# Kernel tuning notes

Hardware: AMD Instinct MI355X
Metric: run time of the kernel (lower is better)

## Reference

```python
import math
import jax, jax.numpy as jnp
import numpy as np

IN_CH = 512
KEY = 512
VAL = 512
B, T = 8, 2048
SQRT_KEY = math.sqrt(float(KEY))


def setup_inputs() -> dict:
    key = jax.random.key(0)
    ks = jax.random.split(key, 7)
    s_in = 1.0 / math.sqrt(IN_CH)
    return {
        "x": jax.random.normal(ks[0], (B, T, IN_CH), dtype=jnp.float32),
        "Wq": jax.random.uniform(ks[1], (IN_CH, KEY), jnp.float32, -s_in, s_in),
        "bq": jax.random.uniform(ks[2], (KEY,), jnp.float32, -s_in, s_in),
        "Wk": jax.random.uniform(ks[3], (IN_CH, KEY), jnp.float32, -s_in, s_in),
        "bk": jax.random.uniform(ks[4], (KEY,), jnp.float32, -s_in, s_in),
        "Wv": jax.random.uniform(ks[5], (IN_CH, VAL), jnp.float32, -s_in, s_in),
        "bv": jax.random.uniform(ks[6], (VAL,), jnp.float32, -s_in, s_in),
    }


def reference(x, Wq, bq, Wk, bk, Wv, bv):
    # x: [B, T, C]
    q = x @ Wq + bq          # [B, T, K]
    k = x @ Wk + bk          # [B, T, K]
    v = x @ Wv + bv          # [B, T, V]
    logits = jnp.einsum("btk,bsk->bts", q, k)  # [B, T(q), T(kv)]
    mask = jnp.tril(jnp.ones((T, T), dtype=bool))  # causal: key s <= query t
    logits = jnp.where(mask[None, :, :], logits, -jnp.inf)
    # NOTE: original torch code softmaxes over dim=1 (the QUERY axis) — kept faithful.
    probs = jax.nn.softmax(logits / SQRT_KEY, axis=1)
    read = jnp.einsum("bts,bsv->btv", probs, v)  # [B, T, V]
    return jnp.concatenate((x, read), axis=2)    # [B, T, C+V]
```

## Files before the change

kernel.cpp:

```cpp
#include <hip/hip_runtime.h>
#include <hip/hip_bf16.h>
#include <math.h>

#define BATCH 8
#define SEQ   2048
#define CH    512
#define ROWS  (BATCH * SEQ)
#define INVSQ 0.044194173824159216f

#define TP 68

typedef __attribute__((ext_vector_type(8))) __bf16 bf16x8;
typedef __attribute__((ext_vector_type(4))) float f32x4;

__device__ inline unsigned short f2bf(float f) {
    unsigned u = __builtin_bit_cast(unsigned, f);
    u += 0x7fffu + ((u >> 16) & 1u);
    return (unsigned short)(u >> 16);
}
__device__ inline float bf2f(unsigned short s) {
    unsigned u = ((unsigned)s) << 16;
    return __builtin_bit_cast(float, u);
}

__global__ __launch_bounds__(256) void fuse_x_kernel(
    const float* __restrict__ x, unsigned short* __restrict__ xb,
    float* __restrict__ out, float* __restrict__ Z)
{
    if (blockIdx.x < 64) Z[blockIdx.x * 256 + threadIdx.x] = 0.f;
    size_t base = ((size_t)blockIdx.x * 256 + threadIdx.x) * 8;
    size_t row = base >> 9, c = base & 511;
    float4 v0 = *(const float4*)(x + base);
    float4 v1 = *(const float4*)(x + base + 4);
    float* o = out + row * 1024 + c;
    *(float4*)o = v0;
    *(float4*)(o + 4) = v1;
    alignas(16) unsigned short t[8];
    t[0] = f2bf(v0.x); t[1] = f2bf(v0.y); t[2] = f2bf(v0.z); t[3] = f2bf(v0.w);
    t[4] = f2bf(v1.x); t[5] = f2bf(v1.y); t[6] = f2bf(v1.z); t[7] = f2bf(v1.w);
    *(uint4*)(xb + base) = *(const uint4*)t;
}

__global__ __launch_bounds__(256) void transpose_w_kernel(
    const float* __restrict__ Wq, const float* __restrict__ Wk,
    const float* __restrict__ Wv, unsigned short* __restrict__ Wt)
{
    __shared__ unsigned short T[64 * TP];
    const int k0 = blockIdx.x * 64, n0 = blockIdx.y * 64, w = blockIdx.z;
    const float* W = (w == 0) ? Wq : (w == 1) ? Wk : Wv;
    const int tid = threadIdx.x;
#pragma unroll
    for (int i = 0; i < 2; ++i) {
        int slot = tid + i * 256;
        int kr = slot >> 3, c8 = (slot & 7) << 3;
        float4 a = *(const float4*)(W + (size_t)(k0 + kr) * CH + n0 + c8);
        float4 b = *(const float4*)(W + (size_t)(k0 + kr) * CH + n0 + c8 + 4);
        T[(c8 + 0) * TP + kr] = f2bf(a.x); T[(c8 + 1) * TP + kr] = f2bf(a.y);
        T[(c8 + 2) * TP + kr] = f2bf(a.z); T[(c8 + 3) * TP + kr] = f2bf(a.w);
        T[(c8 + 4) * TP + kr] = f2bf(b.x); T[(c8 + 5) * TP + kr] = f2bf(b.y);
        T[(c8 + 6) * TP + kr] = f2bf(b.z); T[(c8 + 7) * TP + kr] = f2bf(b.w);
    }
    __syncthreads();
#pragma unroll
    for (int i = 0; i < 2; ++i) {
        int slot = tid + i * 256;
        int nr = slot >> 3, k8 = (slot & 7) << 3;
        uint2 lo = *(const uint2*)(T + nr * TP + k8);
        uint2 hi = *(const uint2*)(T + nr * TP + k8 + 4);
        uint4 u; u.x = lo.x; u.y = lo.y; u.z = hi.x; u.w = hi.y;
        *(uint4*)(Wt + ((size_t)w * CH + n0 + nr) * CH + k0 + k8) = u;
    }
}

__global__ __launch_bounds__(256) void transpose_v_kernel(
    const unsigned short* __restrict__ vb, const float* __restrict__ Z,
    unsigned short* __restrict__ Vt)
{
    __shared__ unsigned short T[64 * TP];
    const int s0 = blockIdx.x * 64, v0 = blockIdx.y * 64, b = blockIdx.z;
    const int tid = threadIdx.x;
#pragma unroll
    for (int i = 0; i < 2; ++i) {
        int slot = tid + i * 256;
        int sr = slot >> 3, c8 = (slot & 7) << 3;
        float inv = 1.0f / Z[b * SEQ + s0 + sr];
        uint4 raw = *(const uint4*)(vb + ((size_t)b * SEQ + s0 + sr) * CH + v0 + c8);
        const unsigned short* p = (const unsigned short*)&raw;
#pragma unroll
        for (int j = 0; j < 8; ++j)
            T[(c8 + j) * TP + sr] = f2bf(bf2f(p[j]) * inv);
    }
    __syncthreads();
#pragma unroll
    for (int i = 0; i < 2; ++i) {
        int slot = tid + i * 256;
        int vr = slot >> 3, s8 = (slot & 7) << 3;
        uint2 lo = *(const uint2*)(T + vr * TP + s8);
        uint2 hi = *(const uint2*)(T + vr * TP + s8 + 4);
        uint4 u; u.x = lo.x; u.y = lo.y; u.z = hi.x; u.w = hi.y;
        *(uint4*)(Vt + ((size_t)b * CH + v0 + vr) * SEQ + s0 + s8) = u;
    }
}

#define FRAG_READS                                                            \
    bf16x8 a0[4], a1[4], c0[4], c1[4];                                        \
    _Pragma("unroll")                                                         \
    for (int rr = 0; rr < 4; ++rr) {                                          \
        const unsigned short* ap = Ab + (arow + rr * 16) * 64;                \
        const unsigned short* bp = Bb + (brow + rr * 16) * 64;                \
        a0[rr] = *(const bf16x8*)(ap + s80);                                  \
        a1[rr] = *(const bf16x8*)(ap + s81);                                  \
        c0[rr] = *(const bf16x8*)(bp + s80);                                  \
        c1[rr] = *(const bf16x8*)(bp + s81);                                  \
    }

#define MFMA_TILE                                                             \
    _Pragma("unroll")                                                         \
    for (int rr = 0; rr < 4; ++rr)                                            \
        _Pragma("unroll")                                                     \
        for (int cc = 0; cc < 4; ++cc)                                        \
            acc[rr][cc] = __builtin_amdgcn_mfma_f32_16x16x32_bf16(            \
                a0[rr], c0[cc], acc[rr][cc], 0, 0, 0);                        \
    _Pragma("unroll")                                                         \
    for (int rr = 0; rr < 4; ++rr)                                            \
        _Pragma("unroll")                                                     \
        for (int cc = 0; cc < 4; ++cc)                                        \
            acc[rr][cc] = __builtin_amdgcn_mfma_f32_16x16x32_bf16(            \
                a1[rr], c1[cc], acc[rr][cc], 0, 0, 0);

#define STAGE4(gsrc, dslab)                                                   \
    _Pragma("unroll")                                                         \
    for (int p = 0; p < 4; ++p)                                               \
        __builtin_amdgcn_global_load_lds(                                     \
            (const __attribute__((address_space(1))) unsigned int*)((gsrc) + (size_t)p * 32 * gstride), \
            (__attribute__((address_space(3))) unsigned int*)((dslab) + p * 2048 + (tid << 3)), \
            16, 0, 0);

#define PIPE_PROLOGUE                                                         \
    stageA(0); stageB(0); stageB(1);                                          \
    asm volatile("s_waitcnt vmcnt(4)" ::: "memory");                          \
    __builtin_amdgcn_s_barrier();                                             \
    __builtin_amdgcn_sched_barrier(0);

#define PIPE_BODY(NTv)                                                        \
    {                                                                         \
        const unsigned short* Ab = lds + (U & 1) * 8192;                      \
        const unsigned short* Bb = lds + 16384 + (U & 1) * 8192;              \
        stageA(U + 1);                                                        \
        FRAG_READS                                                            \
        asm volatile("s_waitcnt lgkmcnt(0)" ::: "memory");                    \
        __builtin_amdgcn_s_barrier();                                         \
        __builtin_amdgcn_sched_barrier(0);                                    \
        stageB(U + 2);                                                        \
        __builtin_amdgcn_s_setprio(1);                                        \
        MFMA_TILE                                                             \
        __builtin_amdgcn_s_setprio(0);                                        \
        if (U <= (NTv) - 3)      asm volatile("s_waitcnt vmcnt(4)" ::: "memory"); \
        else if (U == (NTv) - 2) asm volatile("s_waitcnt vmcnt(0)" ::: "memory"); \
        __builtin_amdgcn_s_barrier();                                         \
        __builtin_amdgcn_sched_barrier(0);                                    \
    }

__global__ __launch_bounds__(256, 2) void qkv8_kernel(
    const unsigned short* __restrict__ xb, const unsigned short* __restrict__ Wt,
    const float* __restrict__ bq, const float* __restrict__ bk,
    const float* __restrict__ bv, unsigned short* __restrict__ qkv)
{
    __shared__ unsigned short lds[32768];
    const int tid = threadIdx.x;
    const int lane = tid & 63, wave = tid >> 6;
    const int waveA = wave >> 1;
    const int waveB = wave & 1;
    const int quad = lane >> 4, l16 = lane & 15;

    int id = (int)blockIdx.x;
    id = (id & 7) * 192 + (id >> 3);
    const int xt = id / 12, wt = id - xt * 12;
    const int xrow0 = xt << 7, wrow0 = wt << 7;

    const size_t gstride = CH;
    const unsigned short* __restrict__ Wg = Wt + (size_t)wrow0 * CH;
    const unsigned short* __restrict__ Xg = xb + (size_t)xrow0 * CH;

    const int scol = (((tid & 7) ^ ((tid >> 3) & 7)) << 3);
    const size_t ga = (size_t)(tid >> 3) * gstride + scol;
    const int s80 = ((quad ^ (l16 & 7)) << 3);
    const int s81 = s80 ^ 32;
    const int arow = waveA * 64 + l16;
    const int brow = waveB * 64 + l16;

    f32x4 acc[4][4] = {};

    auto stageA = [&](int V) {
        if (V >= 8) return;
        const unsigned short* g = Wg + ga + V * 64;
        unsigned short* d = lds + (V & 1) * 8192;
        STAGE4(g, d)
    };
    auto stageB = [&](int V) {
        if (V >= 8) return;
        const unsigned short* g = Xg + ga + V * 64;
        unsigned short* d = lds + 16384 + (V & 1) * 8192;
        STAGE4(g, d)
    };

    PIPE_PROLOGUE
#pragma unroll
    for (int U = 0; U < 8; ++U) PIPE_BODY(8)

    const int which = wrow0 >> 9;
    const float* bias = (which == 0) ? bq : (which == 1) ? bk : bv;
    const float scale = (which == 0) ? INVSQ : 1.0f;
    unsigned short* outw = qkv + (size_t)which * ROWS * CH;
    const int colblk = wrow0 & 511;
#pragma unroll
    for (int r = 0; r < 4; ++r) {
        int colb = colblk + waveA * 64 + r * 16 + quad * 4;
        float4 b4 = *(const float4*)(bias + colb);
#pragma unroll
        for (int c = 0; c < 4; ++c) {
            int m = xrow0 + waveB * 64 + c * 16 + l16;
            alignas(8) unsigned short pk[4];
            pk[0] = f2bf((acc[r][c][0] + b4.x) * scale);
            pk[1] = f2bf((acc[r][c][1] + b4.y) * scale);
            pk[2] = f2bf((acc[r][c][2] + b4.z) * scale);
            pk[3] = f2bf((acc[r][c][3] + b4.w) * scale);
            *(uint2*)(outw + (size_t)m * CH + colb) = *(const uint2*)pk;
        }
    }
}

__global__ __launch_bounds__(256, 2) void logits8_kernel(
    const unsigned short* __restrict__ qb, const unsigned short* __restrict__ kb,
    unsigned short* __restrict__ E, float* __restrict__ Z)
{
    __shared__ unsigned short lds[32768];
    const int tid = threadIdx.x;
    const int lane = tid & 63, wave = tid >> 6;
    const int waveA = wave >> 1;
    const int waveB = wave & 1;
    const int quad = lane >> 4, l16 = lane & 15;

    const int b = (int)blockIdx.x & 7;
    const int i = (int)blockIdx.x >> 3;
    int tt = (int)((sqrtf(8.f * (float)i + 1.f) - 1.f) * 0.5f);
    int st = i - ((tt * (tt + 1)) >> 1);
    while (st < 0)  { --tt; st = i - ((tt * (tt + 1)) >> 1); }
    while (st > tt) { ++tt; st = i - ((tt * (tt + 1)) >> 1); }
    const int m0s = st << 7;
    const int n0t = tt << 7;

    const size_t gstride = CH;
    const unsigned short* __restrict__ Ag = kb + ((size_t)b * SEQ + m0s) * CH;
    const unsigned short* __restrict__ Bg = qb + ((size_t)b * SEQ + n0t) * CH;

    const int scol = (((tid & 7) ^ ((tid >> 3) & 7)) << 3);
    const size_t ga = (size_t)(tid >> 3) * gstride + scol;
    const int s80 = ((quad ^ (l16 & 7)) << 3);
    const int s81 = s80 ^ 32;
    const int arow = waveA * 64 + l16;
    const int brow = waveB * 64 + l16;

    f32x4 acc[4][4] = {};

    auto stageA = [&](int V) {
        if (V >= 8) return;
        const unsigned short* g = Ag + ga + V * 64;
        unsigned short* d = lds + (V & 1) * 8192;
        STAGE4(g, d)
    };
    auto stageB = [&](int V) {
        if (V >= 8) return;
        const unsigned short* g = Bg + ga + V * 64;
        unsigned short* d = lds + 16384 + (V & 1) * 8192;
        STAGE4(g, d)
    };

    PIPE_PROLOGUE
#pragma unroll
    for (int U = 0; U < 8; ++U) PIPE_BODY(8)

#pragma unroll
    for (int r = 0; r < 4; ++r) {
        int sb = m0s + waveA * 64 + r * 16 + quad * 4;
        float ev[4][4];
#pragma unroll
        for (int c = 0; c < 4; ++c) {
            int t = n0t + waveB * 64 + c * 16 + l16;
#pragma unroll
            for (int reg = 0; reg < 4; ++reg)
                ev[c][reg] = (sb + reg <= t) ? __expf(acc[r][c][reg]) : 0.f;
        }
#pragma unroll
        for (int reg = 0; reg < 4; ++reg) {
            float z = ev[0][reg] + ev[1][reg] + ev[2][reg] + ev[3][reg];
            z += __shfl_xor(z, 1);
            z += __shfl_xor(z, 2);
            z += __shfl_xor(z, 4);
            z += __shfl_xor(z, 8);
            if (l16 == 0) atomicAdd(&Z[b * SEQ + sb + reg], z);
        }
#pragma unroll
        for (int c = 0; c < 4; ++c) {
            int t = n0t + waveB * 64 + c * 16 + l16;
            alignas(8) unsigned short pk[4];
            pk[0] = f2bf(ev[c][0]); pk[1] = f2bf(ev[c][1]);
            pk[2] = f2bf(ev[c][2]); pk[3] = f2bf(ev[c][3]);
            *(uint2*)(E + ((size_t)b * SEQ + t) * SEQ + sb) = *(const uint2*)pk;
        }
    }
}

__global__ __launch_bounds__(256, 2) void read8_kernel(
    const unsigned short* __restrict__ E, const unsigned short* __restrict__ Vt,
    float* __restrict__ out)
{
    __shared__ unsigned short lds[32768];
    const int tid = threadIdx.x;
    const int lane = tid & 63, wave = tid >> 6;
    const int waveA = wave >> 1;
    const int waveB = wave & 1;
    const int quad = lane >> 4, l16 = lane & 15;

    const int id = blockIdx.x;
    const int b = id & 7;
    const int rem = id >> 3;
    const int mv = rem & 3;
    const int r0 = rem >> 2;
    const int tt = (r0 < 8) ? r0 : 23 - r0;
    const int m0v = mv << 7;
    const int n0t = tt << 7;
    const int NT = (tt + 1) * 2;

    const size_t gstride = SEQ;
    const unsigned short* __restrict__ Ag = Vt + ((size_t)b * CH + m0v) * SEQ;
    const unsigned short* __restrict__ Bg = E + ((size_t)b * SEQ + n0t) * SEQ;

    const int scol = (((tid & 7) ^ ((tid >> 3) & 7)) << 3);
    const size_t ga = (size_t)(tid >> 3) * gstride + scol;
    const int s80 = ((quad ^ (l16 & 7)) << 3);
    const int s81 = s80 ^ 32;
    const int arow = waveA * 64 + l16;
    const int brow = waveB * 64 + l16;

    f32x4 acc[4][4] = {};

    auto stageA = [&](int V) {
        if (V >= NT) return;
        const unsigned short* g = Ag + ga + V * 64;
        unsigned short* d = lds + (V & 1) * 8192;
        STAGE4(g, d)
    };
    auto stageB = [&](int V) {
        if (V >= NT) return;
        const unsigned short* g = Bg + ga + V * 64;
        unsigned short* d = lds + 16384 + (V & 1) * 8192;
        STAGE4(g, d)
    };

    PIPE_PROLOGUE
#pragma unroll 2
    for (int U = 0; U < NT; ++U) PIPE_BODY(NT)

#pragma unroll
    for (int r = 0; r < 4; ++r) {
        int v = 512 + m0v + waveA * 64 + r * 16 + quad * 4;
#pragma unroll
        for (int c = 0; c < 4; ++c) {
            int t = n0t + waveB * 64 + c * 16 + l16;
            float4 f;
            f.x = acc[r][c][0]; f.y = acc[r][c][1];
            f.z = acc[r][c][2]; f.w = acc[r][c][3];
            *(float4*)(out + ((size_t)b * SEQ + t) * 1024 + v) = f;
        }
    }
}

extern "C" void kernel_launch(void* const* d_in, const int* in_sizes, int n_in,
                              void* d_out, int out_size, void* d_ws, size_t ws_size,
                              hipStream_t stream) {
    const float* x  = (const float*)d_in[0];
    const float* Wq = (const float*)d_in[1];
    const float* bq = (const float*)d_in[2];
    const float* Wk = (const float*)d_in[3];
    const float* bk = (const float*)d_in[4];
    const float* Wv = (const float*)d_in[5];
    const float* bv = (const float*)d_in[6];
    float* out = (float*)d_out;

    char* ws = (char*)d_ws;
    const size_t QKV_BYTES = (size_t)ROWS * CH * 2;
    const size_t E_BYTES   = (size_t)BATCH * SEQ * SEQ * 2;
    unsigned short* qkv = (unsigned short*)ws;
    unsigned short* qb = qkv;
    unsigned short* kb = (unsigned short*)(ws + QKV_BYTES);
    unsigned short* vb = (unsigned short*)(ws + 2 * QKV_BYTES);
    unsigned short* E  = (unsigned short*)(ws + 3 * QKV_BYTES);
    float* Z = (float*)(ws + 3 * QKV_BYTES + E_BYTES);
    unsigned short* xb = E;
    unsigned short* Wt = (unsigned short*)((char*)E + QKV_BYTES);
    unsigned short* Vt = qb;

    dim3 blk(256);
    fuse_x_kernel<<<dim3(4096), blk, 0, stream>>>(x, xb, out, Z);
    transpose_w_kernel<<<dim3(8, 8, 3), blk, 0, stream>>>(Wq, Wk, Wv, Wt);
    qkv8_kernel<<<dim3(1536), blk, 0, stream>>>(xb, Wt, bq, bk, bv, qkv);
    logits8_kernel<<<dim3(1088), blk, 0, stream>>>(qb, kb, E, Z);
    transpose_v_kernel<<<dim3(32, 8, 8), blk, 0, stream>>>(vb, Z, Vt);
    read8_kernel<<<dim3(512), blk, 0, stream>>>(E, Vt, out);
}
```

Before: 213.9 us.

## Triple-buffer B operand in LDS and drop mid-iteration barrier in GEMM pipeline

The B operand staging buffer goes from two LDS slots to three (indexed by U % 3) in all three GEMM kernels. This lets stageB(U+2) be issued at the top of each iteration without overwriting data still being read, so the mid-iteration s_barrier can be removed. Fragment reads are split into two halves with a partial lgkmcnt wait, so the first half of the MFMAs can start while the second-half LDS reads are still in flight. The cost is more LDS per block (64KB to 80KB), which could limit occupancy, and modulo-3 indexing.

```diff
diff --git a/kernel.cpp b/kernel.cpp
--- a/kernel.cpp
+++ b/kernel.cpp
@@ -102,32 +102,6 @@
     }
 }
 
-#define FRAG_READS                                                            \
-    bf16x8 a0[4], a1[4], c0[4], c1[4];                                        \
-    _Pragma("unroll")                                                         \
-    for (int rr = 0; rr < 4; ++rr) {                                          \
-        const unsigned short* ap = Ab + (arow + rr * 16) * 64;                \
-        const unsigned short* bp = Bb + (brow + rr * 16) * 64;                \
-        a0[rr] = *(const bf16x8*)(ap + s80);                                  \
-        a1[rr] = *(const bf16x8*)(ap + s81);                                  \
-        c0[rr] = *(const bf16x8*)(bp + s80);                                  \
-        c1[rr] = *(const bf16x8*)(bp + s81);                                  \
-    }
-
-#define MFMA_TILE                                                             \
-    _Pragma("unroll")                                                         \
-    for (int rr = 0; rr < 4; ++rr)                                            \
-        _Pragma("unroll")                                                     \
-        for (int cc = 0; cc < 4; ++cc)                                        \
-            acc[rr][cc] = __builtin_amdgcn_mfma_f32_16x16x32_bf16(            \
-                a0[rr], c0[cc], acc[rr][cc], 0, 0, 0);                        \
-    _Pragma("unroll")                                                         \
-    for (int rr = 0; rr < 4; ++rr)                                            \
-        _Pragma("unroll")                                                     \
-        for (int cc = 0; cc < 4; ++cc)                                        \
-            acc[rr][cc] = __builtin_amdgcn_mfma_f32_16x16x32_bf16(            \
-                a1[rr], c1[cc], acc[rr][cc], 0, 0, 0);
-
 #define STAGE4(gsrc, dslab)                                                   \
     _Pragma("unroll")                                                         \
     for (int p = 0; p < 4; ++p)                                               \
@@ -145,15 +119,40 @@
 #define PIPE_BODY(NTv)                                                        \
     {                                                                         \
         const unsigned short* Ab = lds + (U & 1) * 8192;                      \
-        const unsigned short* Bb = lds + 16384 + (U & 1) * 8192;              \
+        const unsigned short* Bb = lds + 16384 + (U % 3) * 8192;              \
         stageA(U + 1);                                                        \
-        FRAG_READS                                                            \
+        stageB(U + 2);                                                        \
+        bf16x8 a0[4], a1[4], c0[4], c1[4];                                    \
+        _Pragma("unroll")                                                     \
+        for (int rr = 0; rr < 4; ++rr) {                                      \
+            a0[rr] = *(const bf16x8*)(Ab + (arow + rr * 16) * 64 + s80);      \
+            c0[rr] = *(const bf16x8*)(Bb + (brow + rr * 16) * 64 + s80);      \
+        }                                                                     \
+        __builtin_amdgcn_sched_barrier(0);                                    \
+        _Pragma("unroll")                                                     \
+        for (int rr = 0; rr < 4; ++rr) {                                      \
+            a1[rr] = *(const bf16x8*)(Ab + (arow + rr * 16) * 64 + s81);      \
+            c1[rr] = *(const bf16x8*)(Bb + (brow + rr * 16) * 64 + s81);      \
+        }                                                                     \
+        asm volatile("s_waitcnt lgkmcnt(8)" ::: "memory");                    \
+        __builtin_amdgcn_sched_barrier(0);                                    \
+        __builtin_amdgcn_s_setprio(1);                                        \
+        _Pragma("unroll")                                                     \
+        for (int rr = 0; rr < 4; ++rr)                                        \
+            _Pragma("unroll")                                                 \
+            for (int cc = 0; cc < 4; ++cc)                                    \
+                acc[rr][cc] = __builtin_amdgcn_mfma_f32_16x16x32_bf16(        \
+                    a0[rr], c0[cc], acc[rr][cc], 0, 0, 0);                    \
+        __builtin_amdgcn_s_setprio(0);                                        \
         asm volatile("s_waitcnt lgkmcnt(0)" ::: "memory");                    \
-        __builtin_amdgcn_s_barrier();                                         \
         __builtin_amdgcn_sched_barrier(0);                                    \
-        stageB(U + 2);                                                        \
         __builtin_amdgcn_s_setprio(1);                                        \
-        MFMA_TILE                                                             \
+        _Pragma("unroll")                                                     \
+        for (int rr = 0; rr < 4; ++rr)                                        \
+            _Pragma("unroll")                                                 \
+            for (int cc = 0; cc < 4; ++cc)                                    \
+                acc[rr][cc] = __builtin_amdgcn_mfma_f32_16x16x32_bf16(        \
+                    a1[rr], c1[cc], acc[rr][cc], 0, 0, 0);                    \
         __builtin_amdgcn_s_setprio(0);                                        \
         if (U <= (NTv) - 3)      asm volatile("s_waitcnt vmcnt(4)" ::: "memory"); \
         else if (U == (NTv) - 2) asm volatile("s_waitcnt vmcnt(0)" ::: "memory"); \
@@ -166,7 +165,7 @@
     const float* __restrict__ bq, const float* __restrict__ bk,
     const float* __restrict__ bv, unsigned short* __restrict__ qkv)
 {
-    __shared__ unsigned short lds[32768];
+    __shared__ unsigned short lds[40960];
     const int tid = threadIdx.x;
     const int lane = tid & 63, wave = tid >> 6;
     const int waveA = wave >> 1;
@@ -200,7 +199,7 @@
     auto stageB = [&](int V) {
         if (V >= 8) return;
         const unsigned short* g = Xg + ga + V * 64;
-        unsigned short* d = lds + 16384 + (V & 1) * 8192;
+        unsigned short* d = lds + 16384 + (V % 3) * 8192;
         STAGE4(g, d)
     };
 
@@ -234,7 +233,7 @@
     const unsigned short* __restrict__ qb, const unsigned short* __restrict__ kb,
     unsigned short* __restrict__ E, float* __restrict__ Z)
 {
-    __shared__ unsigned short lds[32768];
+    __shared__ unsigned short lds[40960];
     const int tid = threadIdx.x;
     const int lane = tid & 63, wave = tid >> 6;
     const int waveA = wave >> 1;
@@ -272,7 +271,7 @@
     auto stageB = [&](int V) {
         if (V >= 8) return;
         const unsigned short* g = Bg + ga + V * 64;
-        unsigned short* d = lds + 16384 + (V & 1) * 8192;
+        unsigned short* d = lds + 16384 + (V % 3) * 8192;
         STAGE4(g, d)
     };
 
@@ -315,7 +314,7 @@
     const unsigned short* __restrict__ E, const unsigned short* __restrict__ Vt,
     float* __restrict__ out)
 {
-    __shared__ unsigned short lds[32768];
+    __shared__ unsigned short lds[40960];
     const int tid = threadIdx.x;
     const int lane = tid & 63, wave = tid >> 6;
     const int waveA = wave >> 1;
@@ -354,7 +353,7 @@
     auto stageB = [&](int V) {
         if (V >= NT) return;
         const unsigned short* g = Bg + ga + V * 64;
-        unsigned short* d = lds + 16384 + (V & 1) * 8192;
+        unsigned short* d = lds + 16384 + (V % 3) * 8192;
         STAGE4(g, d)
     };
 
```

Measured after the change: 214.3 us. Within noise of the previous version (+0.2%).

## Enlarge QKV and logits GEMM tiles to 256x256 with 8 waves

Applied to the files above, without the earlier changes.

The qkv and logits GEMM kernels move from 128x128 tiles with 4 waves to 256x256 tiles with 512 threads and 8 waves. Each wave now owns a 128x64 output, and the inner loop is split into four MFMA sub-steps with barriers between them. This raises arithmetic intensity and cuts block count, at the cost of 128KB of LDS, more accumulator registers and more barriers per K step. The read kernel gets a triple-buffered B stage and split fragment reads with partial lgkmcnt waits, so MFMAs can start before all LDS reads finish.

```diff
diff --git a/kernel.cpp b/kernel.cpp
--- a/kernel.cpp
+++ b/kernel.cpp
@@ -102,111 +102,126 @@
     }
 }
 
-#define FRAG_READS                                                            \
-    bf16x8 a0[4], a1[4], c0[4], c1[4];                                        \
-    _Pragma("unroll")                                                         \
-    for (int rr = 0; rr < 4; ++rr) {                                          \
-        const unsigned short* ap = Ab + (arow + rr * 16) * 64;                \
-        const unsigned short* bp = Bb + (brow + rr * 16) * 64;                \
-        a0[rr] = *(const bf16x8*)(ap + s80);                                  \
-        a1[rr] = *(const bf16x8*)(ap + s81);                                  \
-        c0[rr] = *(const bf16x8*)(bp + s80);                                  \
-        c1[rr] = *(const bf16x8*)(bp + s81);                                  \
-    }
-
-#define MFMA_TILE                                                             \
-    _Pragma("unroll")                                                         \
-    for (int rr = 0; rr < 4; ++rr)                                            \
-        _Pragma("unroll")                                                     \
-        for (int cc = 0; cc < 4; ++cc)                                        \
-            acc[rr][cc] = __builtin_amdgcn_mfma_f32_16x16x32_bf16(            \
-                a0[rr], c0[cc], acc[rr][cc], 0, 0, 0);                        \
-    _Pragma("unroll")                                                         \
-    for (int rr = 0; rr < 4; ++rr)                                            \
-        _Pragma("unroll")                                                     \
-        for (int cc = 0; cc < 4; ++cc)                                        \
-            acc[rr][cc] = __builtin_amdgcn_mfma_f32_16x16x32_bf16(            \
-                a1[rr], c1[cc], acc[rr][cc], 0, 0, 0);
-
 #define STAGE4(gsrc, dslab)                                                   \
     _Pragma("unroll")                                                         \
     for (int p = 0; p < 4; ++p)                                               \
         __builtin_amdgcn_global_load_lds(                                     \
-            (const __attribute__((address_space(1))) unsigned int*)((gsrc) + (size_t)p * 32 * gstride), \
-            (__attribute__((address_space(3))) unsigned int*)((dslab) + p * 2048 + (tid << 3)), \
+            (const __attribute__((address_space(1))) unsigned int*)((gsrc) + (size_t)p * 64 * gstride), \
+            (__attribute__((address_space(3))) unsigned int*)((dslab) + p * 4096 + (tid << 3)), \
             16, 0, 0);
 
-#define PIPE_PROLOGUE                                                         \
-    stageA(0); stageB(0); stageB(1);                                          \
-    asm volatile("s_waitcnt vmcnt(4)" ::: "memory");                          \
+#define RD_A(rb)                                                              \
+    a00 = *(const bf16x8*)(Ab + (arow + (rb)     * 16) * 64 + s80);           \
+    a01 = *(const bf16x8*)(Ab + (arow + (rb)     * 16) * 64 + s81);           \
+    a10 = *(const bf16x8*)(Ab + (arow + (rb + 1) * 16) * 64 + s80);           \
+    a11 = *(const bf16x8*)(Ab + (arow + (rb + 1) * 16) * 64 + s81);
+
+#define MFMA_PAIR(rb)                                                         \
+    __builtin_amdgcn_s_setprio(1);                                            \
+    _Pragma("unroll")                                                         \
+    for (int cc = 0; cc < 4; ++cc)                                            \
+        acc[rb][cc] = __builtin_amdgcn_mfma_f32_16x16x32_bf16(a00, b0[cc], acc[rb][cc], 0, 0, 0); \
+    _Pragma("unroll")                                                         \
+    for (int cc = 0; cc < 4; ++cc)                                            \
+        acc[(rb) + 1][cc] = __builtin_amdgcn_mfma_f32_16x16x32_bf16(a10, b0[cc], acc[(rb) + 1][cc], 0, 0, 0); \
+    _Pragma("unroll")                                                         \
+    for (int cc = 0; cc < 4; ++cc)                                            \
+        acc[rb][cc] = __builtin_amdgcn_mfma_f32_16x16x32_bf16(a01, b1[cc], acc[rb][cc], 0, 0, 0); \
+    _Pragma("unroll")                                                         \
+    for (int cc = 0; cc < 4; ++cc)                                            \
+        acc[(rb) + 1][cc] = __builtin_amdgcn_mfma_f32_16x16x32_bf16(a11, b1[cc], acc[(rb) + 1][cc], 0, 0, 0); \
+    __builtin_amdgcn_s_setprio(0);
+
+#define BAR_LGKM                                                              \
     __builtin_amdgcn_s_barrier();                                             \
+    asm volatile("s_waitcnt lgkmcnt(0)" ::: "memory");                        \
     __builtin_amdgcn_sched_barrier(0);
 
-#define PIPE_BODY(NTv)                                                        \
-    {                                                                         \
-        const unsigned short* Ab = lds + (U & 1) * 8192;                      \
-        const unsigned short* Bb = lds + 16384 + (U & 1) * 8192;              \
+#define PIPE256(NT)                                                           \
+    stageA(0); stageB(0);                                                     \
+    asm volatile("s_waitcnt vmcnt(0)" ::: "memory");                          \
+    __builtin_amdgcn_s_barrier();                                             \
+    __builtin_amdgcn_sched_barrier(0);                                        \
+    _Pragma("unroll")                                                         \
+    for (int U = 0; U < (NT); ++U) {                                          \
+        const unsigned short* Ab = lds + (U & 1) * 16384;                     \
+        const unsigned short* Bb = lds + 32768 + (U & 1) * 16384;             \
+        bf16x8 b0[4], b1[4], a00, a01, a10, a11;                              \
+                                                            \
         stageA(U + 1);                                                        \
-        FRAG_READS                                                            \
-        asm volatile("s_waitcnt lgkmcnt(0)" ::: "memory");                    \
+        _Pragma("unroll")                                                     \
+        for (int n = 0; n < 4; ++n) {                                         \
+            b0[n] = *(const bf16x8*)(Bb + (brow + n * 16) * 64 + s80);        \
+            b1[n] = *(const bf16x8*)(Bb + (brow + n * 16) * 64 + s81);        \
+        }                                                                     \
+        RD_A(0)                                                               \
+        BAR_LGKM                                                              \
+        MFMA_PAIR(0)                                                          \
+        __builtin_amdgcn_s_barrier();                                         \
+                                                            \
+        stageB(U + 1);                                                        \
+        RD_A(2)                                                               \
+        BAR_LGKM                                                              \
+        MFMA_PAIR(2)                                                          \
+        __builtin_amdgcn_s_barrier();                                         \
+                                                            \
+        RD_A(4)                                                               \
+        BAR_LGKM                                                              \
+        MFMA_PAIR(4)                                                          \
+        __builtin_amdgcn_s_barrier();                                         \
+                                                            \
+        RD_A(6)                                                               \
+        BAR_LGKM                                                              \
+        MFMA_PAIR(6)                                                          \
+        if (U <= (NT) - 2) asm volatile("s_waitcnt vmcnt(0)" ::: "memory");   \
         __builtin_amdgcn_s_barrier();                                         \
         __builtin_amdgcn_sched_barrier(0);                                    \
-        stageB(U + 2);                                                        \
-        __builtin_amdgcn_s_setprio(1);                                        \
-        MFMA_TILE                                                             \
-        __builtin_amdgcn_s_setprio(0);                                        \
-        if (U <= (NTv) - 3)      asm volatile("s_waitcnt vmcnt(4)" ::: "memory"); \
-        else if (U == (NTv) - 2) asm volatile("s_waitcnt vmcnt(0)" ::: "memory"); \
-        __builtin_amdgcn_s_barrier();                                         \
-        __builtin_amdgcn_sched_barrier(0);                                    \
-    }
-
-__global__ __launch_bounds__(256, 2) void qkv8_kernel(
+    }
+
+__global__ __launch_bounds__(512) void qkv8_kernel(
     const unsigned short* __restrict__ xb, const unsigned short* __restrict__ Wt,
     const float* __restrict__ bq, const float* __restrict__ bk,
     const float* __restrict__ bv, unsigned short* __restrict__ qkv)
 {
-    __shared__ unsigned short lds[32768];
+    __shared__ unsigned short lds[65536];
     const int tid = threadIdx.x;
     const int lane = tid & 63, wave = tid >> 6;
-    const int waveA = wave >> 1;
-    const int waveB = wave & 1;
+    const int waveA = wave >> 2;
+    const int waveB = wave & 3;
     const int quad = lane >> 4, l16 = lane & 15;
 
     int id = (int)blockIdx.x;
-    id = (id & 7) * 192 + (id >> 3);
-    const int xt = id / 12, wt = id - xt * 12;
-    const int xrow0 = xt << 7, wrow0 = wt << 7;
+    id = (id & 7) * 48 + (id >> 3);
+    const int xt = id / 6, wt = id - xt * 6;
+    const int xrow0 = xt << 8, wrow0 = wt << 8;
 
     const size_t gstride = CH;
-    const unsigned short* __restrict__ Wg = Wt + (size_t)wrow0 * CH;
-    const unsigned short* __restrict__ Xg = xb + (size_t)xrow0 * CH;
+    const unsigned short* __restrict__ Ag = Wt + (size_t)wrow0 * CH;
+    const unsigned short* __restrict__ Bg = xb + (size_t)xrow0 * CH;
 
     const int scol = (((tid & 7) ^ ((tid >> 3) & 7)) << 3);
     const size_t ga = (size_t)(tid >> 3) * gstride + scol;
     const int s80 = ((quad ^ (l16 & 7)) << 3);
     const int s81 = s80 ^ 32;
-    const int arow = waveA * 64 + l16;
+    const int arow = waveA * 128 + l16;
     const int brow = waveB * 64 + l16;
 
-    f32x4 acc[4][4] = {};
+    f32x4 acc[8][4] = {};
 
     auto stageA = [&](int V) {
         if (V >= 8) return;
-        const unsigned short* g = Wg + ga + V * 64;
-        unsigned short* d = lds + (V & 1) * 8192;
+        const unsigned short* g = Ag + ga + V * 64;
+        unsigned short* d = lds + (V & 1) * 16384;
         STAGE4(g, d)
     };
     auto stageB = [&](int V) {
         if (V >= 8) return;
-        const unsigned short* g = Xg + ga + V * 64;
-        unsigned short* d = lds + 16384 + (V & 1) * 8192;
+        const unsigned short* g = Bg + ga + V * 64;
+        unsigned short* d = lds + 32768 + (V & 1) * 16384;
         STAGE4(g, d)
     };
 
-    PIPE_PROLOGUE
-#pragma unroll
-    for (int U = 0; U < 8; ++U) PIPE_BODY(8)
+    PIPE256(8)
 
     const int which = wrow0 >> 9;
     const float* bias = (which == 0) ? bq : (which == 1) ? bk : bv;
@@ -214,8 +229,8 @@
     unsigned short* outw = qkv + (size_t)which * ROWS * CH;
     const int colblk = wrow0 & 511;
 #pragma unroll
-    for (int r = 0; r < 4; ++r) {
-        int colb = colblk + waveA * 64 + r * 16 + quad * 4;
+    for (int r = 0; r < 8; ++r) {
+        int colb = colblk + waveA * 128 + r * 16 + quad * 4;
         float4 b4 = *(const float4*)(bias + colb);
 #pragma unroll
         for (int c = 0; c < 4; ++c) {
@@ -230,15 +245,15 @@
     }
 }
 
-__global__ __launch_bounds__(256, 2) void logits8_kernel(
+__global__ __launch_bounds__(512) void logits8_kernel(
     const unsigned short* __restrict__ qb, const unsigned short* __restrict__ kb,
     unsigned short* __restrict__ E, float* __restrict__ Z)
 {
-    __shared__ unsigned short lds[32768];
+    __shared__ unsigned short lds[65536];
     const int tid = threadIdx.x;
     const int lane = tid & 63, wave = tid >> 6;
-    const int waveA = wave >> 1;
-    const int waveB = wave & 1;
+    const int waveA = wave >> 2;
+    const int waveB = wave & 3;
     const int quad = lane >> 4, l16 = lane & 15;
 
     const int b = (int)blockIdx.x & 7;
@@ -247,8 +262,8 @@
     int st = i - ((tt * (tt + 1)) >> 1);
     while (st < 0)  { --tt; st = i - ((tt * (tt + 1)) >> 1); }
     while (st > tt) { ++tt; st = i - ((tt * (tt + 1)) >> 1); }
-    const int m0s = st << 7;
-    const int n0t = tt << 7;
+    const int m0s = st << 8;
+    const int n0t = tt << 8;
 
     const size_t gstride = CH;
     const unsigned short* __restrict__ Ag = kb + ((size_t)b * SEQ + m0s) * CH;
@@ -258,31 +273,29 @@
     const size_t ga = (size_t)(tid >> 3) * gstride + scol;
     const int s80 = ((quad ^ (l16 & 7)) << 3);
     const int s81 = s80 ^ 32;
-    const int arow = waveA * 64 + l16;
+    const int arow = waveA * 128 + l16;
     const int brow = waveB * 64 + l16;
 
-    f32x4 acc[4][4] = {};
+    f32x4 acc[8][4] = {};
 
     auto stageA = [&](int V) {
         if (V >= 8) return;
         const unsigned short* g = Ag + ga + V * 64;
-        unsigned short* d = lds + (V & 1) * 8192;
+        unsigned short* d = lds + (V & 1) * 16384;
         STAGE4(g, d)
     };
     auto stageB = [&](int V) {
         if (V >= 8) return;
         const unsigned short* g = Bg + ga + V * 64;
-        unsigned short* d = lds + 16384 + (V & 1) * 8192;
+        unsigned short* d = lds + 32768 + (V & 1) * 16384;
         STAGE4(g, d)
     };
 
-    PIPE_PROLOGUE
-#pragma unroll
-    for (int U = 0; U < 8; ++U) PIPE_BODY(8)
-
-#pragma unroll
-    for (int r = 0; r < 4; ++r) {
-        int sb = m0s + waveA * 64 + r * 16 + quad * 4;
+    PIPE256(8)
+
+#pragma unroll
+    for (int r = 0; r < 8; ++r) {
+        int sb = m0s + waveA * 128 + r * 16 + quad * 4;
         float ev[4][4];
 #pragma unroll
         for (int c = 0; c < 4; ++c) {
@@ -311,11 +324,19 @@
     }
 }
 
+#define R_STAGE4(gsrc, dslab)                                                 \
+    _Pragma("unroll")                                                         \
+    for (int p = 0; p < 4; ++p)                                               \
+        __builtin_amdgcn_global_load_lds(                                     \
+            (const __attribute__((address_space(1))) unsigned int*)((gsrc) + (size_t)p * 32 * gstride), \
+            (__attribute__((address_space(3))) unsigned int*)((dslab) + p * 2048 + (tid << 3)), \
+            16, 0, 0);
+
 __global__ __launch_bounds__(256, 2) void read8_kernel(
     const unsigned short* __restrict__ E, const unsigned short* __restrict__ Vt,
     float* __restrict__ out)
 {
-    __shared__ unsigned short lds[32768];
+    __shared__ unsigned short lds[40960];
     const int tid = threadIdx.x;
     const int lane = tid & 63, wave = tid >> 6;
     const int waveA = wave >> 1;
@@ -349,18 +370,63 @@
         if (V >= NT) return;
         const unsigned short* g = Ag + ga + V * 64;
         unsigned short* d = lds + (V & 1) * 8192;
-        STAGE4(g, d)
+        R_STAGE4(g, d)
     };
     auto stageB = [&](int V) {
         if (V >= NT) return;
         const unsigned short* g = Bg + ga + V * 64;
-        unsigned short* d = lds + 16384 + (V & 1) * 8192;
-        STAGE4(g, d)
-    };
-
-    PIPE_PROLOGUE
+        unsigned short* d = lds + 16384 + (V % 3) * 8192;
+        R_STAGE4(g, d)
+    };
+
+    stageA(0); stageB(0); stageB(1);
+    asm volatile("s_waitcnt vmcnt(4)" ::: "memory");
+    __builtin_amdgcn_s_barrier();
+    __builtin_amdgcn_sched_barrier(0);
+
 #pragma unroll 2
-    for (int U = 0; U < NT; ++U) PIPE_BODY(NT)
+    for (int U = 0; U < NT; ++U) {
+        const unsigned short* Ab = lds + (U & 1) * 8192;
+        const unsigned short* Bb = lds + 16384 + (U % 3) * 8192;
+        stageA(U + 1);
+        stageB(U + 2);
+        bf16x8 a0[4], a1[4], c0[4], c1[4];
+#pragma unroll
+        for (int rr = 0; rr < 4; ++rr) {
+            a0[rr] = *(const bf16x8*)(Ab + (arow + rr * 16) * 64 + s80);
+            c0[rr] = *(const bf16x8*)(Bb + (brow + rr * 16) * 64 + s80);
+        }
+        __builtin_amdgcn_sched_barrier(0);
+#pragma unroll
+        for (int rr = 0; rr < 4; ++rr) {
+            a1[rr] = *(const bf16x8*)(Ab + (arow + rr * 16) * 64 + s81);
+            c1[rr] = *(const bf16x8*)(Bb + (brow + rr * 16) * 64 + s81);
+        }
+        asm volatile("s_waitcnt lgkmcnt(8)" ::: "memory");
+        __builtin_amdgcn_sched_barrier(0);
+        __builtin_amdgcn_s_setprio(1);
+#pragma unroll
+        for (int rr = 0; rr < 4; ++rr)
+#pragma unroll
+            for (int cc = 0; cc < 4; ++cc)
+                acc[rr][cc] = __builtin_amdgcn_mfma_f32_16x16x32_bf16(
+                    a0[rr], c0[cc], acc[rr][cc], 0, 0, 0);
+        __builtin_amdgcn_s_setprio(0);
+        asm volatile("s_waitcnt lgkmcnt(0)" ::: "memory");
+        __builtin_amdgcn_sched_barrier(0);
+        __builtin_amdgcn_s_setprio(1);
+#pragma unroll
+        for (int rr = 0; rr < 4; ++rr)
+#pragma unroll
+            for (int cc = 0; cc < 4; ++cc)
+                acc[rr][cc] = __builtin_amdgcn_mfma_f32_16x16x32_bf16(
+                    a1[rr], c1[cc], acc[rr][cc], 0, 0, 0);
+        __builtin_amdgcn_s_setprio(0);
+        if (U <= NT - 3)      asm volatile("s_waitcnt vmcnt(4)" ::: "memory");
+        else if (U == NT - 2) asm volatile("s_waitcnt vmcnt(0)" ::: "memory");
+        __builtin_amdgcn_s_barrier();
+        __builtin_amdgcn_sched_barrier(0);
+    }
 
 #pragma unroll
     for (int r = 0; r < 4; ++r) {
@@ -404,8 +470,8 @@
     dim3 blk(256);
     fuse_x_kernel<<<dim3(4096), blk, 0, stream>>>(x, xb, out, Z);
     transpose_w_kernel<<<dim3(8, 8, 3), blk, 0, stream>>>(Wq, Wk, Wv, Wt);
-    qkv8_kernel<<<dim3(1536), blk, 0, stream>>>(xb, Wt, bq, bk, bv, qkv);
-    logits8_kernel<<<dim3(1088), blk, 0, stream>>>(qb, kb, E, Z);
+    qkv8_kernel<<<dim3(384), dim3(512), 0, stream>>>(xb, Wt, bq, bk, bv, qkv);
+    logits8_kernel<<<dim3(288), dim3(512), 0, stream>>>(qb, kb, E, Z);
     transpose_v_kernel<<<dim3(32, 8, 8), blk, 0, stream>>>(vb, Z, Vt);
     read8_kernel<<<dim3(512), blk, 0, stream>>>(E, Vt, out);
 }
```

Result: slower. 230.7 us (+7.8%).
